# Optimization experiments

Hardware: AMD Instinct MI355X
Metric: run time of the kernel (lower is better)

The kernel has to match this reference:

```python
import jax, jax.numpy as jnp
import numpy as np

B, L, D = 1, 2048, 2048
NH, NKV, HD = 32, 8, 64          # heads, kv heads, head_dim = D // NH
THETA = 50000.0
EPS = 1e-5
SCALE = HD ** -0.5


def _rope(x):
    # traditional (interleaved-pair) RoPE; x: (B, H, L, HD)
    hd = x.shape[-1]
    pos = jnp.arange(x.shape[2], dtype=jnp.float32)
    inv = THETA ** (-jnp.arange(0, hd, 2, dtype=jnp.float32) / hd)
    ang = pos[:, None] * inv[None, :]              # (L, HD/2)
    cos, sin = jnp.cos(ang), jnp.sin(ang)
    x1, x2 = x[..., ::2], x[..., 1::2]
    r1 = x1 * cos - x2 * sin
    r2 = x1 * sin + x2 * cos
    return jnp.stack([r1, r2], axis=-1).reshape(x.shape)


def _rmsnorm(x, w):
    return x * jax.lax.rsqrt(jnp.mean(x * x, axis=-1, keepdims=True) + EPS) * w


def setup_inputs() -> dict:
    key = jax.random.key(0)
    ks = jax.random.split(key, 5)
    x = jax.random.normal(ks[0], (B, L, D), dtype=jnp.float32)
    w_qkv = jax.random.normal(ks[1], (NH * HD + 2 * NKV * HD, D), dtype=jnp.float32) * 0.02
    w_out = jax.random.normal(ks[2], (D, D), dtype=jnp.float32) * 0.02
    q_gamma = 1.0 + 0.02 * jax.random.normal(ks[3], (HD,), dtype=jnp.float32)
    k_gamma = 1.0 + 0.02 * jax.random.normal(ks[4], (HD,), dtype=jnp.float32)
    mask = jnp.tril(jnp.ones((L, L), dtype=bool))   # causal
    return {"x": x, "w_qkv": w_qkv, "w_out": w_out,
            "q_gamma": q_gamma, "k_gamma": k_gamma, "mask": mask}


def reference(x, w_qkv, w_out, q_gamma, k_gamma, mask):
    b, l, d = x.shape
    qkv = x @ w_qkv.T                               # fused QKV proj (no bias)
    q, k, v = jnp.split(qkv, [NH * HD, NH * HD + NKV * HD], axis=-1)
    q = q.reshape(b, l, NH, HD).transpose(0, 2, 1, 3)     # (B,NH,L,HD)
    k = k.reshape(b, l, NKV, HD).transpose(0, 2, 1, 3)    # (B,NKV,L,HD)
    v = v.reshape(b, l, NKV, HD).transpose(0, 2, 1, 3)
    q = _rmsnorm(_rope(q), q_gamma)
    k = _rmsnorm(_rope(k), k_gamma)
    g = NH // NKV                                   # GQA group size
    qg = q.reshape(b, NKV, g, l, HD)
    scores = jnp.einsum('bkgqd,bkld->bkgql', qg, k) * SCALE
    scores = jnp.where(mask, scores, -jnp.inf)
    attn = jax.nn.softmax(scores, axis=-1)
    out = jnp.einsum('bkgql,bkld->bkgqd', attn, v)  # (B,NKV,g,L,HD)
    out = out.reshape(b, NH, l, HD).transpose(0, 2, 1, 3).reshape(b, l, d)
    return out @ w_out.T
```

## Files before the change

### kernel.cpp

```cpp
#include <hip/hip_runtime.h>

using bf16   = __bf16;
using bf16x4 = __bf16 __attribute__((ext_vector_type(4)));
using bf16x8 = __bf16 __attribute__((ext_vector_type(8)));
using f32x4  = float __attribute__((ext_vector_type(4)));
using f32x16 = float __attribute__((ext_vector_type(16)));
using u32x2  = unsigned int __attribute__((ext_vector_type(2)));
using u32x4  = unsigned int __attribute__((ext_vector_type(4)));

#define L_SEQ  2048
#define DMODEL 2048
#define NQH    32
#define NKVH   8
#define HDIM   64
#define QKV_N  3072

#define KVF_HSTRIDE (64 * 4 * 64 * 8)

#define FIXED_M 16.0f

__device__ __forceinline__ void gload_lds16(const void* g, void* lds) {
  __builtin_amdgcn_global_load_lds((__attribute__((address_space(1))) void*)(g),
                                   (__attribute__((address_space(3))) void*)(lds),
                                   16, 0, 0);
}

__device__ __forceinline__ unsigned pack2(float a, float b) {
  union { bf16 h[2]; unsigned u; } x;
  x.h[0] = (bf16)a; x.h[1] = (bf16)b;
  return x.u;
}

__device__ __forceinline__ bf16x8 make_pfrag(float p0, float p1, float p2, float p3,
                                             float p4, float p5, float p6, float p7,
                                             int hi) {
  const unsigned W0 = pack2(p0, p1);
  const unsigned W1 = pack2(p2, p3);
  const unsigned W2 = pack2(p4, p5);
  const unsigned W3 = pack2(p6, p7);
  u32x4 pw;
#if __has_builtin(__builtin_amdgcn_permlane32_swap)
  {
    using i32x2 = int __attribute__((ext_vector_type(2)));
    const i32x2 r02 = __builtin_amdgcn_permlane32_swap((int)W0, (int)W2, false, false);
    const i32x2 r13 = __builtin_amdgcn_permlane32_swap((int)W1, (int)W3, false, false);
    pw = u32x4{ (unsigned)r02[0], (unsigned)r13[0], (unsigned)r02[1], (unsigned)r13[1] };
  }
#else
  {
    const unsigned X0 = (unsigned)__shfl_xor((int)W0, 32);
    const unsigned X1 = (unsigned)__shfl_xor((int)W1, 32);
    const unsigned X2 = (unsigned)__shfl_xor((int)W2, 32);
    const unsigned X3 = (unsigned)__shfl_xor((int)W3, 32);
    pw = u32x4{ hi ? X2 : W0, hi ? X3 : W1, hi ? W2 : X0, hi ? W3 : X1 };
  }
#endif
  return __builtin_bit_cast(bf16x8, pw);
}

__device__ __forceinline__ int chunk_base64(int Qb) {
  return (Qb < 8)  ? Qb
       : (Qb < 16) ? 8  + 2 * (Qb - 8)
       : (Qb < 24) ? 24 + 3 * (Qb - 16)
                   : 48 + 4 * (Qb - 24);
}

#define N4_X  (L_SEQ * DMODEL / 4)
#define N4_WQ (QKV_N * DMODEL / 4)
#define N4_WO (DMODEL * DMODEL / 4)
__global__ void cvt3_f32_bf16(const float* __restrict__ x, const float* __restrict__ wq,
                              const float* __restrict__ wo, bf16* __restrict__ xb,
                              bf16* __restrict__ wqb, bf16* __restrict__ wob) {
  const long stride = (long)gridDim.x * blockDim.x;
  const long ntot = N4_X + N4_WQ + N4_WO;
  for (long i = (long)blockIdx.x * blockDim.x + threadIdx.x; i < ntot; i += stride) {
    const float* src; bf16* dst; long j;
    if (i < N4_X)               { src = x;  dst = xb;  j = i; }
    else if (i < N4_X + N4_WQ)  { src = wq; dst = wqb; j = i - N4_X; }
    else                        { src = wo; dst = wob; j = i - N4_X - N4_WQ; }
    const float4 v = reinterpret_cast<const float4*>(src)[j];
    bf16x4 o = { (bf16)v.x, (bf16)v.y, (bf16)v.z, (bf16)v.w };
    reinterpret_cast<bf16x4*>(dst)[j] = o;
  }
}

template <typename OutT>
__global__ __launch_bounds__(128)
void gemm_bt(const bf16* __restrict__ A, const bf16* __restrict__ B,
             OutT* __restrict__ C, int M, int N, int K) {
  __shared__ bf16 As[128 * 64];
  __shared__ bf16 Bs[64 * 64];
  const int tid = threadIdx.x;
  const int w = tid >> 6, l = tid & 63;
  const int lq = l & 15, lg = l >> 4;
  const long m0 = (long)blockIdx.y * 128;
  const long n0 = (long)blockIdx.x * 64;
  const int ks = K / gridDim.z;
  const int kb = blockIdx.z * ks;
  C += (long)blockIdx.z * M * N;

  const int lrow = l >> 3;
  const int scol = ((l & 7) ^ lrow) << 3;

  f32x4 acc[4][4];
#pragma unroll
  for (int i = 0; i < 4; ++i)
#pragma unroll
    for (int j = 0; j < 4; ++j) acc[i][j] = f32x4{0.f, 0.f, 0.f, 0.f};

  for (int k0 = kb; k0 < kb + ks; k0 += 64) {
#pragma unroll
    for (int i = 0; i < 8; ++i) {
      const int r0 = (i * 2 + w) * 8;
      gload_lds16(A + (m0 + r0 + lrow) * (long)K + k0 + scol, &As[r0 * 64]);
    }
#pragma unroll
    for (int i = 0; i < 4; ++i) {
      const int r0 = (i * 2 + w) * 8;
      gload_lds16(B + (n0 + r0 + lrow) * (long)K + k0 + scol, &Bs[r0 * 64]);
    }
    __syncthreads();
#pragma unroll
    for (int kk = 0; kk < 2; ++kk) {
      bf16x8 af[4], bfr[4];
#pragma unroll
      for (int t = 0; t < 4; ++t) {
        const int rowA = w * 64 + t * 16 + lq;
        const int blkA = (kk * 4 + lg) ^ (rowA & 7);
        af[t] = *reinterpret_cast<const bf16x8*>(&As[rowA * 64 + blkA * 8]);
        const int rowB = t * 16 + lq;
        const int blkB = (kk * 4 + lg) ^ (rowB & 7);
        bfr[t] = *reinterpret_cast<const bf16x8*>(&Bs[rowB * 64 + blkB * 8]);
      }
#pragma unroll
      for (int mt = 0; mt < 4; ++mt)
#pragma unroll
        for (int nt = 0; nt < 4; ++nt)
          acc[mt][nt] = __builtin_amdgcn_mfma_f32_16x16x32_bf16(af[mt], bfr[nt], acc[mt][nt], 0, 0, 0);
    }
    __syncthreads();
  }

#pragma unroll
  for (int mt = 0; mt < 4; ++mt)
#pragma unroll
    for (int r = 0; r < 4; ++r) {
      const long row = m0 + w * 64 + mt * 16 + lg * 4 + r;
#pragma unroll
      for (int nt = 0; nt < 4; ++nt) {
        const long col = n0 + nt * 16 + lq;
        C[row * (long)N + col] = (OutT)acc[mt][nt][r];
      }
    }
}

__global__ __launch_bounds__(256)
void rope_repack(const bf16* __restrict__ pA, const bf16* __restrict__ pB,
                 const float* __restrict__ qg, const float* __restrict__ kg,
                 bf16* __restrict__ qo, bf16* __restrict__ kfr, bf16* __restrict__ vfr) {
  __shared__ bf16 t[32][72];
  if (blockIdx.x < 20480) {
    const int gid = blockIdx.x * 4 + (threadIdx.x >> 6);
    const int lane = threadIdx.x & 63;
    const int pos = gid / 40;
    const int hh = gid % 40;
    const bool isq = hh < 32;
    const int col = isq ? hh * HDIM : NQH * HDIM + (hh - 32) * HDIM;

    const long idx = (long)pos * QKV_N + col + lane;
    float x = (float)pA[idx] + (float)pB[idx];
    float p = __shfl_xor(x, 1);
    const float fi = (float)(lane & ~1) * (1.0f / 64.0f);
    const float inv = powf(50000.0f, -fi);
    const float ang = (float)pos * inv;
    const float sn = sinf(ang), cs = cosf(ang);
    const float r = (lane & 1) ? (p * sn + x * cs) : (x * cs - p * sn);

    float ss = r * r;
#pragma unroll
    for (int off = 1; off < 64; off <<= 1) ss += __shfl_xor(ss, off);
    const float scl = rsqrtf(ss * (1.0f / 64.0f) + 1e-5f);
    const float g = isq ? qg[lane] : kg[lane];
    const float o = r * scl * g;

    if (isq) {
      qo[(long)pos * DMODEL + hh * HDIM + lane] = (bf16)(o * 0.18033688011112042f);
    } else {
      const int kvh = hh - 32;
      const int d = lane;
      const int lp = (pos & 31) + (((d >> 3) & 1) << 5);
      const long kidx = ((((long)kvh * 64 + (pos >> 5)) * 4 + (d >> 4)) * 64 + lp) * 8 + (d & 7);
      kfr[kidx] = (bf16)o;
    }
  } else {
    const int bid = blockIdx.x - 20480;
    const int kvh = bid >> 6;
    const int kb = bid & 63;
    const int tid = threadIdx.x;
    {
      const int row = tid >> 3;
      const int cc = (tid & 7) * 8;
      const long goff = (long)(kb * 32 + row) * QKV_N + (NQH * HDIM + NKVH * HDIM) + kvh * HDIM + cc;
      const bf16x8 a = *reinterpret_cast<const bf16x8*>(pA + goff);
      const bf16x8 b = *reinterpret_cast<const bf16x8*>(pB + goff);
      bf16x8 s;
#pragma unroll
      for (int e = 0; e < 8; ++e) s[e] = (bf16)((float)a[e] + (float)b[e]);
      *reinterpret_cast<bf16x8*>(&t[row][cc]) = s;
    }
    __syncthreads();

    const int f = tid >> 6, l = tid & 63;
    const int s = f >> 1, dh = f & 1;
    const int hi = l >> 5, l31 = l & 31;
    union { bf16 b[8]; u32x4 u; } o;
#pragma unroll
    for (int e = 0; e < 8; ++e) o.b[e] = t[s * 16 + hi * 8 + e][dh * 32 + l31];
    bf16* od = vfr + (((long)(kvh * 64 + kb) * 4 + f) * 64 + l) * 8;
    *reinterpret_cast<u32x4*>(od) = o.u;
  }
}

__global__ __launch_bounds__(256, 2)
void flash_attn(const bf16* __restrict__ Q, const bf16* __restrict__ Kfr,
                const bf16* __restrict__ Vfr,
                bf16* __restrict__ po, float* __restrict__ pl, bf16* __restrict__ ao) {
  const int w = threadIdx.x >> 6, l = threadIdx.x & 63;
  const int lane31 = l & 31, hi = l >> 5;
  const int bb = blockIdx.x;
  const int kvh = bb & 7;
  const int g = 79 - (bb >> 3);

  int Qb, c;
  if (g < 8)       { Qb = g;                   c = 0; }
  else if (g < 24) { Qb = 8 + ((g - 8) >> 1);  c = (g - 8) & 1; }
  else if (g < 48) { Qb = 16 + (g - 24) / 3;   c = (g - 24) % 3; }
  else             { Qb = 24 + ((g - 48) >> 2); c = (g - 48) & 3; }

  const int h = kvh * 4 + w;
  const int s0 = c * 16;
  const int s1 = min(2 * Qb + 2, s0 + 16);
  const int pidx = h * 80 + g;

  const int q0A = Qb * 64;
  const int qA = q0A + lane31;
  const int qB = q0A + 32 + lane31;
  const int l8 = l * 8;

  const bf16* kfrh = Kfr + (long)kvh * KVF_HSTRIDE;
  const bf16* vfrh = Vfr + (long)kvh * KVF_HSTRIDE;

  const bf16* qrowA = Q + (long)qA * DMODEL + h * HDIM + hi * 8;
  const bf16* qrowB = Q + (long)qB * DMODEL + h * HDIM + hi * 8;
  bf16x8 qfA[4], qfB[4];
#pragma unroll
  for (int cc = 0; cc < 4; ++cc) {
    qfA[cc] = *reinterpret_cast<const bf16x8*>(qrowA + cc * 16);
    qfB[cc] = *reinterpret_cast<const bf16x8*>(qrowB + cc * 16);
  }

  f32x16 oA0, oA1, oB0, oB1;
#pragma unroll
  for (int r = 0; r < 16; ++r) { oA0[r] = 0.f; oA1[r] = 0.f; oB0[r] = 0.f; oB1[r] = 0.f; }
  float lsA = 0.f, lsB = 0.f;

  bf16x8 kc0, kc1, kc2, kc3;
  {
    const bf16* kp = kfrh + (long)s0 * 2048 + l8;
    kc0 = *reinterpret_cast<const bf16x8*>(kp);
    kc1 = *reinterpret_cast<const bf16x8*>(kp + 512);
    kc2 = *reinterpret_cast<const bf16x8*>(kp + 1024);
    kc3 = *reinterpret_cast<const bf16x8*>(kp + 1536);
  }

  for (int sti = s0; sti < s1; ++sti) {
    const int kb0 = sti * 32;

    const bf16* vp = vfrh + (long)sti * 2048 + l8;
    const bf16x8 va0 = *reinterpret_cast<const bf16x8*>(vp);
    const bf16x8 vb0 = *reinterpret_cast<const bf16x8*>(vp + 512);
    const bf16x8 va1 = *reinterpret_cast<const bf16x8*>(vp + 1024);
    const bf16x8 vb1 = *reinterpret_cast<const bf16x8*>(vp + 1536);

    const long knoff = (sti + 1 < s1) ? (long)(sti + 1) * 2048 : (long)s0 * 2048;
    const bf16* kp = kfrh + knoff + l8;
    const bf16x8 kn0 = *reinterpret_cast<const bf16x8*>(kp);
    const bf16x8 kn1 = *reinterpret_cast<const bf16x8*>(kp + 512);
    const bf16x8 kn2 = *reinterpret_cast<const bf16x8*>(kp + 1024);
    const bf16x8 kn3 = *reinterpret_cast<const bf16x8*>(kp + 1536);

    if (kb0 <= q0A + 31) {
      f32x16 st;
#pragma unroll
      for (int r = 0; r < 16; ++r) st[r] = 0.f;
      st = __builtin_amdgcn_mfma_f32_32x32x16_bf16(kc0, qfA[0], st, 0, 0, 0);
      st = __builtin_amdgcn_mfma_f32_32x32x16_bf16(kc1, qfA[1], st, 0, 0, 0);
      st = __builtin_amdgcn_mfma_f32_32x32x16_bf16(kc2, qfA[2], st, 0, 0, 0);
      st = __builtin_amdgcn_mfma_f32_32x32x16_bf16(kc3, qfA[3], st, 0, 0, 0);

      if (kb0 + 31 > q0A) {
#pragma unroll
        for (int r = 0; r < 16; ++r) {
          const int k_abs = kb0 + (r & 3) + 8 * (r >> 2) + 4 * hi;
          if (k_abs > qA) st[r] = -3.0e38f;
        }
      }

      float rs = 0.f;
#pragma unroll
      for (int r = 0; r < 16; ++r) { st[r] = __builtin_amdgcn_exp2f(st[r] - FIXED_M); rs += st[r]; }
      rs += __shfl_xor(rs, 32);
      lsA += rs;

      const bf16x8 pf0 = make_pfrag(st[0], st[1], st[2], st[3], st[4], st[5], st[6], st[7], hi);
      oA0 = __builtin_amdgcn_mfma_f32_32x32x16_bf16(va0, pf0, oA0, 0, 0, 0);
      oA1 = __builtin_amdgcn_mfma_f32_32x32x16_bf16(vb0, pf0, oA1, 0, 0, 0);
      const bf16x8 pf1 = make_pfrag(st[8], st[9], st[10], st[11], st[12], st[13], st[14], st[15], hi);
      oA0 = __builtin_amdgcn_mfma_f32_32x32x16_bf16(va1, pf1, oA0, 0, 0, 0);
      oA1 = __builtin_amdgcn_mfma_f32_32x32x16_bf16(vb1, pf1, oA1, 0, 0, 0);
    }

    {
      f32x16 st;
#pragma unroll
      for (int r = 0; r < 16; ++r) st[r] = 0.f;
      st = __builtin_amdgcn_mfma_f32_32x32x16_bf16(kc0, qfB[0], st, 0, 0, 0);
      st = __builtin_amdgcn_mfma_f32_32x32x16_bf16(kc1, qfB[1], st, 0, 0, 0);
      st = __builtin_amdgcn_mfma_f32_32x32x16_bf16(kc2, qfB[2], st, 0, 0, 0);
      st = __builtin_amdgcn_mfma_f32_32x32x16_bf16(kc3, qfB[3], st, 0, 0, 0);

      if (kb0 + 31 > q0A + 32) {
#pragma unroll
        for (int r = 0; r < 16; ++r) {
          const int k_abs = kb0 + (r & 3) + 8 * (r >> 2) + 4 * hi;
          if (k_abs > qB) st[r] = -3.0e38f;
        }
      }

      float rs = 0.f;
#pragma unroll
      for (int r = 0; r < 16; ++r) { st[r] = __builtin_amdgcn_exp2f(st[r] - FIXED_M); rs += st[r]; }
      rs += __shfl_xor(rs, 32);
      lsB += rs;

      const bf16x8 pf0 = make_pfrag(st[0], st[1], st[2], st[3], st[4], st[5], st[6], st[7], hi);
      oB0 = __builtin_amdgcn_mfma_f32_32x32x16_bf16(va0, pf0, oB0, 0, 0, 0);
      oB1 = __builtin_amdgcn_mfma_f32_32x32x16_bf16(vb0, pf0, oB1, 0, 0, 0);
      const bf16x8 pf1 = make_pfrag(st[8], st[9], st[10], st[11], st[12], st[13], st[14], st[15], hi);
      oB0 = __builtin_amdgcn_mfma_f32_32x32x16_bf16(va1, pf1, oB0, 0, 0, 0);
      oB1 = __builtin_amdgcn_mfma_f32_32x32x16_bf16(vb1, pf1, oB1, 0, 0, 0);
    }

    kc0 = kn0; kc1 = kn1; kc2 = kn2; kc3 = kn3;
  }

  if (g < 8) {
    const float rlA = 1.0f / lsA, rlB = 1.0f / lsB;
    bf16* orowA = ao + (long)qA * DMODEL + h * HDIM;
    bf16* orowB = ao + (long)qB * DMODEL + h * HDIM;
#pragma unroll
    for (int gg = 0; gg < 4; ++gg) {
      const int d0 = 8 * gg + 4 * hi;
      u32x2 a0 = { pack2(oA0[4 * gg + 0] * rlA, oA0[4 * gg + 1] * rlA),
                   pack2(oA0[4 * gg + 2] * rlA, oA0[4 * gg + 3] * rlA) };
      u32x2 a1 = { pack2(oA1[4 * gg + 0] * rlA, oA1[4 * gg + 1] * rlA),
                   pack2(oA1[4 * gg + 2] * rlA, oA1[4 * gg + 3] * rlA) };
      *reinterpret_cast<u32x2*>(orowA + d0) = a0;
      *reinterpret_cast<u32x2*>(orowA + 32 + d0) = a1;
      u32x2 b0 = { pack2(oB0[4 * gg + 0] * rlB, oB0[4 * gg + 1] * rlB),
                   pack2(oB0[4 * gg + 2] * rlB, oB0[4 * gg + 3] * rlB) };
      u32x2 b1 = { pack2(oB1[4 * gg + 0] * rlB, oB1[4 * gg + 1] * rlB),
                   pack2(oB1[4 * gg + 2] * rlB, oB1[4 * gg + 3] * rlB) };
      *reinterpret_cast<u32x2*>(orowB + d0) = b0;
      *reinterpret_cast<u32x2*>(orowB + 32 + d0) = b1;
    }
  } else {
    bf16* pbase = po + (long)pidx * 4096;
#pragma unroll
    for (int gg = 0; gg < 4; ++gg) {
      const int d0 = 8 * gg + 4 * hi;
      u32x2 a0 = { pack2(oA0[4 * gg + 0], oA0[4 * gg + 1]),
                   pack2(oA0[4 * gg + 2], oA0[4 * gg + 3]) };
      u32x2 a1 = { pack2(oA1[4 * gg + 0], oA1[4 * gg + 1]),
                   pack2(oA1[4 * gg + 2], oA1[4 * gg + 3]) };
      *reinterpret_cast<u32x2*>(pbase + lane31 * 64 + d0) = a0;
      *reinterpret_cast<u32x2*>(pbase + lane31 * 64 + 32 + d0) = a1;
      u32x2 b0 = { pack2(oB0[4 * gg + 0], oB0[4 * gg + 1]),
                   pack2(oB0[4 * gg + 2], oB0[4 * gg + 3]) };
      u32x2 b1 = { pack2(oB1[4 * gg + 0], oB1[4 * gg + 1]),
                   pack2(oB1[4 * gg + 2], oB1[4 * gg + 3]) };
      *reinterpret_cast<u32x2*>(pbase + (32 + lane31) * 64 + d0) = b0;
      *reinterpret_cast<u32x2*>(pbase + (32 + lane31) * 64 + 32 + d0) = b1;
    }
    if (hi == 0) {
      pl[pidx * 64 + lane31] = lsA;
      pl[pidx * 64 + 32 + lane31] = lsB;
    }
  }
}

__global__ __launch_bounds__(256)
void combine_split(const bf16* __restrict__ po, const float* __restrict__ pl,
                   bf16* __restrict__ ao) {
  const int t = blockIdx.x;
  const int tid = threadIdx.x;
  const int r = tid >> 2;
  const int dc = (tid & 3) * 16;
  const int h = t / 24;
  const int Qb = 8 + (t % 24);
  const int nc = (Qb < 16) ? 2 : (Qb < 24) ? 3 : 4;
  const int p0 = h * 80 + chunk_base64(Qb);

  float lv = pl[(p0 + 0) * 64 + r] + pl[(p0 + 1) * 64 + r];
  if (nc > 2) lv += pl[(p0 + 2) * 64 + r];
  if (nc > 3) lv += pl[(p0 + 3) * 64 + r];
  const float invL = 1.0f / lv;

  float acc[16];
#pragma unroll
  for (int j = 0; j < 16; ++j) acc[j] = 0.f;

#pragma unroll
  for (int c = 0; c < 4; ++c) {
    if (c < nc) {
      const bf16* src = po + ((long)(p0 + c) * 4096) + r * 64 + dc;
      const bf16x8 a0 = *reinterpret_cast<const bf16x8*>(src);
      const bf16x8 a1 = *reinterpret_cast<const bf16x8*>(src + 8);
#pragma unroll
      for (int j = 0; j < 8; ++j) {
        acc[j]     += (float)a0[j];
        acc[8 + j] += (float)a1[j];
      }
    }
  }

  const long q_abs = (long)Qb * 64 + r;
  bf16* od = ao + q_abs * DMODEL + h * HDIM + dc;
  union { bf16 b[16]; u32x4 u[2]; } o;
#pragma unroll
  for (int j = 0; j < 16; ++j) o.b[j] = (bf16)(acc[j] * invL);
  *reinterpret_cast<u32x4*>(od) = o.u[0];
  *reinterpret_cast<u32x4*>(od + 8) = o.u[1];
}

extern "C" void kernel_launch(void* const* d_in, const int* in_sizes, int n_in,
                              void* d_out, int out_size, void* d_ws, size_t ws_size,
                              hipStream_t stream) {
  const float* x       = (const float*)d_in[0];
  const float* w_qkv   = (const float*)d_in[1];
  const float* w_out   = (const float*)d_in[2];
  const float* q_gamma = (const float*)d_in[3];
  const float* k_gamma = (const float*)d_in[4];

  char* ws = (char*)d_ws;
  bf16* xb    = (bf16*)(ws);
  bf16* wqb   = (bf16*)(ws + (8ul  << 20));
  bf16* wob   = (bf16*)(ws + (20ul << 20));
  bf16* qkvpA = (bf16*)(ws + (28ul << 20));
  bf16* qkvpB = (bf16*)(ws + (40ul << 20));
  bf16* qb    = (bf16*)(ws);
  bf16* kfr   = (bf16*)(ws + (8ul  << 20));
  bf16* vfr   = (bf16*)(ws + (10ul << 20));
  bf16* po    = (bf16*)(ws + (28ul << 20));
  float* pl   = (float*)(ws + (48ul << 20));
  bf16* ao    = (bf16*)(ws + (52ul << 20));
  float* out  = (float*)d_out;

  cvt3_f32_bf16<<<2048, 256, 0, stream>>>(x, w_qkv, w_out, xb, wqb, wob);

  gemm_bt<bf16><<<dim3(QKV_N / 64, L_SEQ / 128, 2), 128, 0, stream>>>(xb, wqb, qkvpA, L_SEQ, QKV_N, DMODEL);

  rope_repack<<<20992, 256, 0, stream>>>(qkvpA, qkvpB, q_gamma, k_gamma, qb, kfr, vfr);

  flash_attn<<<640, 256, 0, stream>>>(qb, kfr, vfr, po, pl, ao);
  combine_split<<<768, 256, 0, stream>>>(po, pl, ao);

  gemm_bt<float><<<dim3(DMODEL / 64, L_SEQ / 128, 1), 128, 0, stream>>>(ao, wob, out, L_SEQ, DMODEL, DMODEL);
}
```

Before: 162.5 us.

## Drop split-K in QKV GEMM and add XCD-aware workgroup swizzle

The QKV projection GEMM no longer splits K across two partial outputs. The rope/repack kernel therefore reads a single bf16 QKV buffer instead of summing two partials, which removes one partial write and one partial read. Both GEMMs now remap the workgroup id so that consecutive tiles are grouped by id modulo 8, meant to improve L2 locality across XCDs. The trade-off is that the QKV GEMM launches half as many workgroups (768 instead of 1536), each doing twice the K work. The single bf16 rounding of the full sum also changes numerics slightly.

```diff
diff --git a/kernel.cpp b/kernel.cpp
--- a/kernel.cpp
+++ b/kernel.cpp
@@ -93,11 +93,14 @@
   const int tid = threadIdx.x;
   const int w = tid >> 6, l = tid & 63;
   const int lq = l & 15, lg = l >> 4;
-  const long m0 = (long)blockIdx.y * 128;
-  const long n0 = (long)blockIdx.x * 64;
-  const int ks = K / gridDim.z;
-  const int kb = blockIdx.z * ks;
-  C += (long)blockIdx.z * M * N;
+
+  const int nwg = gridDim.x * gridDim.y;
+  const int wgid = blockIdx.y * gridDim.x + blockIdx.x;
+  const int swz = (wgid & 7) * (nwg >> 3) + (wgid >> 3);
+  const int bx = swz % gridDim.x;
+  const int by = swz / gridDim.x;
+  const long m0 = (long)by * 128;
+  const long n0 = (long)bx * 64;
 
   const int lrow = l >> 3;
   const int scol = ((l & 7) ^ lrow) << 3;
@@ -108,7 +111,7 @@
 #pragma unroll
     for (int j = 0; j < 4; ++j) acc[i][j] = f32x4{0.f, 0.f, 0.f, 0.f};
 
-  for (int k0 = kb; k0 < kb + ks; k0 += 64) {
+  for (int k0 = 0; k0 < K; k0 += 64) {
 #pragma unroll
     for (int i = 0; i < 8; ++i) {
       const int r0 = (i * 2 + w) * 8;
@@ -155,7 +158,7 @@
 }
 
 __global__ __launch_bounds__(256)
-void rope_repack(const bf16* __restrict__ pA, const bf16* __restrict__ pB,
+void rope_repack(const bf16* __restrict__ qkv,
                  const float* __restrict__ qg, const float* __restrict__ kg,
                  bf16* __restrict__ qo, bf16* __restrict__ kfr, bf16* __restrict__ vfr) {
   __shared__ bf16 t[32][72];
@@ -167,8 +170,7 @@
     const bool isq = hh < 32;
     const int col = isq ? hh * HDIM : NQH * HDIM + (hh - 32) * HDIM;
 
-    const long idx = (long)pos * QKV_N + col + lane;
-    float x = (float)pA[idx] + (float)pB[idx];
+    float x = (float)qkv[(long)pos * QKV_N + col + lane];
     float p = __shfl_xor(x, 1);
     const float fi = (float)(lane & ~1) * (1.0f / 64.0f);
     const float inv = powf(50000.0f, -fi);
@@ -201,12 +203,7 @@
       const int row = tid >> 3;
       const int cc = (tid & 7) * 8;
       const long goff = (long)(kb * 32 + row) * QKV_N + (NQH * HDIM + NKVH * HDIM) + kvh * HDIM + cc;
-      const bf16x8 a = *reinterpret_cast<const bf16x8*>(pA + goff);
-      const bf16x8 b = *reinterpret_cast<const bf16x8*>(pB + goff);
-      bf16x8 s;
-#pragma unroll
-      for (int e = 0; e < 8; ++e) s[e] = (bf16)((float)a[e] + (float)b[e]);
-      *reinterpret_cast<bf16x8*>(&t[row][cc]) = s;
+      *reinterpret_cast<bf16x8*>(&t[row][cc]) = *reinterpret_cast<const bf16x8*>(qkv + goff);
     }
     __syncthreads();
 
@@ -456,8 +453,7 @@
   bf16* xb    = (bf16*)(ws);
   bf16* wqb   = (bf16*)(ws + (8ul  << 20));
   bf16* wob   = (bf16*)(ws + (20ul << 20));
-  bf16* qkvpA = (bf16*)(ws + (28ul << 20));
-  bf16* qkvpB = (bf16*)(ws + (40ul << 20));
+  bf16* qkv   = (bf16*)(ws + (28ul << 20));
   bf16* qb    = (bf16*)(ws);
   bf16* kfr   = (bf16*)(ws + (8ul  << 20));
   bf16* vfr   = (bf16*)(ws + (10ul << 20));
@@ -468,12 +464,12 @@
 
   cvt3_f32_bf16<<<2048, 256, 0, stream>>>(x, w_qkv, w_out, xb, wqb, wob);
 
-  gemm_bt<bf16><<<dim3(QKV_N / 64, L_SEQ / 128, 2), 128, 0, stream>>>(xb, wqb, qkvpA, L_SEQ, QKV_N, DMODEL);
-
-  rope_repack<<<20992, 256, 0, stream>>>(qkvpA, qkvpB, q_gamma, k_gamma, qb, kfr, vfr);
+  gemm_bt<bf16><<<dim3(QKV_N / 64, L_SEQ / 128), 128, 0, stream>>>(xb, wqb, qkv, L_SEQ, QKV_N, DMODEL);
+
+  rope_repack<<<20992, 256, 0, stream>>>(qkv, q_gamma, k_gamma, qb, kfr, vfr);
 
   flash_attn<<<640, 256, 0, stream>>>(qb, kfr, vfr, po, pl, ao);
   combine_split<<<768, 256, 0, stream>>>(po, pl, ao);
 
-  gemm_bt<float><<<dim3(DMODEL / 64, L_SEQ / 128, 1), 128, 0, stream>>>(ao, wob, out, L_SEQ, DMODEL, DMODEL);
-}
+  gemm_bt<float><<<dim3(DMODEL / 64, L_SEQ / 128), 128, 0, stream>>>(ao, wob, out, L_SEQ, DMODEL, DMODEL);
+}
```

After: 164.4 us. Within noise of the previous version (+1.2%).
